# Kernel optimization log

Measured on AMD Instinct MI355X. Metric: run time of the kernel, lower is better.

The kernel has to match this reference:

```python
import jax, jax.numpy as jnp
import numpy as np

LENGTHSCALE = 0.3
EPS = 1e-10
N = 100000   # evaluation points
M = 3375     # grid_size**3 RBF centers


def setup_inputs() -> dict:
    key = jax.random.key(0)
    k1, k2, k3, k4, k5 = jax.random.split(key, 5)
    x = jax.random.normal(k1, (N, 3), dtype=jnp.float32)
    centers = jax.random.normal(k2, (M, 3), dtype=jnp.float32)
    coeff_u = jax.random.normal(k3, (M,), dtype=jnp.float32)
    coeff_v = jax.random.normal(k4, (M,), dtype=jnp.float32)
    coeff_w = jax.random.normal(k5, (M,), dtype=jnp.float32)
    return {"x": x, "centers": centers, "coeff_u": coeff_u,
            "coeff_v": coeff_v, "coeff_w": coeff_w}


def reference(x, centers, coeff_u, coeff_v, coeff_w):
    # base sphere-attractor field: x * (1 - ||x||)
    r = jnp.linalg.norm(x, axis=-1, keepdims=True)          # (N, 1)
    base = x * (1.0 - r)                                    # (N, 3)

    x_sq = jnp.sum(x * x, axis=-1, keepdims=True)           # (N, 1)
    c_sq = jnp.sum(centers * centers, axis=-1)[None, :]     # (1, M)
    xy = x @ centers.T                                      # (N, M)
    dist2 = jnp.maximum(x_sq + c_sq - 2.0 * xy, EPS)        # (N, M)

    # RBF features and three shared-phi matvecs fused as one matmul
    phi = jnp.exp(-dist2 / (2.0 * LENGTHSCALE ** 2))        # (N, M)
    coeffs = jnp.stack([coeff_u, coeff_v, coeff_w], axis=1) # (M, 3)
    uvw = phi @ coeffs                                      # (N, 3)
    return base + uvw
```

## Files before the change

kernel.cpp:

```cpp
#include <hip/hip_runtime.h>
#include <hip/hip_bf16.h>

#define S2 8.014973f
#define K2 16.029946f
#define NCHUNK 21

typedef float f2 __attribute__((ext_vector_type(2)));

__global__ void rbf_prep_kernel(const float* __restrict__ centers,
                                const float* __restrict__ cu,
                                const float* __restrict__ cv,
                                const float* __restrict__ cw,
                                float4* __restrict__ cpack, int M) {
    int m = blockIdx.x * 256 + threadIdx.x;
    if (m < M) {
        float cx = centers[3 * m + 0];
        float cy = centers[3 * m + 1];
        float cz = centers[3 * m + 2];
        float4 a, b;
        a.x = K2 * cx;
        a.y = K2 * cy;
        a.z = K2 * cz;
        a.w = -S2 * (cx * cx + cy * cy + cz * cz);
        b.x = cu[m];
        b.y = cv[m];
        b.z = cw[m];
        b.w = 0.f;
        cpack[2 * m + 0] = a;
        cpack[2 * m + 1] = b;
    }
}

__global__ __launch_bounds__(256) void rbf_main_kernel(
    const float* __restrict__ x, const float4* __restrict__ cpack,
    float* __restrict__ out, int N, int M, int NT, int per, int ntask) {
    const int tid = threadIdx.x;
    const int lane = tid & 63;
    const int wave0 =
        __builtin_amdgcn_readfirstlane(blockIdx.x * 4 + (tid >> 6));
    const int nwaves = gridDim.x * 4;

    for (int task = wave0; task < ntask; task += nwaves) {
        const int tile = task % NT;
        const int chunk = task / NT;
        const int p0 = tile * 128 + lane;
        const int p1 = p0 + 64;

        float x00 = 0.f, x01 = 0.f, x02 = 0.f;
        float x10 = 0.f, x11 = 0.f, x12 = 0.f;
        if (p0 < N) {
            x00 = x[3 * p0 + 0];
            x01 = x[3 * p0 + 1];
            x02 = x[3 * p0 + 2];
        }
        if (p1 < N) {
            x10 = x[3 * p1 + 0];
            x11 = x[3 * p1 + 1];
            x12 = x[3 * p1 + 2];
        }

        const f2 X = {x00, x10};
        const f2 Y = {x01, x11};
        const f2 Z = {x02, x12};
        const f2 PX = {-S2 * (x00 * x00 + x01 * x01 + x02 * x02),
                       -S2 * (x10 * x10 + x11 * x11 + x12 * x12)};

        const int jb = chunk * per;
        const int je = min(jb + per, M);

        f2 au = {0.f, 0.f}, av = {0.f, 0.f}, aw = {0.f, 0.f};

#pragma unroll 4
        for (int j = jb; j < je; ++j) {
            const float4 a = cpack[2 * j + 0];
            const float4 b = cpack[2 * j + 1];
            f2 e = PX + a.w;
            e += Z * a.z;
            e += Y * a.y;
            e += X * a.x;
            f2 phi;
            phi.x = __builtin_amdgcn_exp2f(e.x);
            phi.y = __builtin_amdgcn_exp2f(e.y);
            au += phi * b.x;
            av += phi * b.y;
            aw += phi * b.z;
        }

        if (chunk == 0) {
            float g0 = 1.f - sqrtf(x00 * x00 + x01 * x01 + x02 * x02);
            au.x += x00 * g0;
            av.x += x01 * g0;
            aw.x += x02 * g0;
            float g1 = 1.f - sqrtf(x10 * x10 + x11 * x11 + x12 * x12);
            au.y += x10 * g1;
            av.y += x11 * g1;
            aw.y += x12 * g1;
        }

        if (p0 < N) {
            atomicAdd(&out[3 * p0 + 0], au.x);
            atomicAdd(&out[3 * p0 + 1], av.x);
            atomicAdd(&out[3 * p0 + 2], aw.x);
        }
        if (p1 < N) {
            atomicAdd(&out[3 * p1 + 0], au.y);
            atomicAdd(&out[3 * p1 + 1], av.y);
            atomicAdd(&out[3 * p1 + 2], aw.y);
        }
    }
}

extern "C" void kernel_launch(void* const* d_in, const int* in_sizes, int n_in,
                              void* d_out, int out_size, void* d_ws,
                              size_t ws_size, hipStream_t stream) {
    const float* x = (const float*)d_in[0];
    const float* centers = (const float*)d_in[1];
    const float* cu = (const float*)d_in[2];
    const float* cv = (const float*)d_in[3];
    const float* cw = (const float*)d_in[4];
    const int N = in_sizes[0] / 3;
    const int M = in_sizes[1] / 3;
    float4* cpack = (float4*)d_ws;
    float* out = (float*)d_out;

    const int NT = (N + 127) / 128;
    const int per = (M + NCHUNK - 1) / NCHUNK;
    const int ntask = NT * NCHUNK;

    hipLaunchKernelGGL(rbf_prep_kernel, dim3((M + 255) / 256), dim3(256), 0,
                       stream, centers, cu, cv, cw, cpack, M);
    hipMemsetAsync(d_out, 0, (size_t)out_size * sizeof(float), stream);
    hipLaunchKernelGGL(rbf_main_kernel, dim3(2048), dim3(256), 0, stream, x,
                       cpack, out, N, M, NT, per, ntask);
}
```

Measured before the change: 146.8 us.

## Load center data via scalar prefetch and process four points per lane

Replaces per-lane vector loads of the packed center data with inline-asm scalar s_load_dwordx16, double-buffered so the next pair of centers loads while the current pair is computed. Each lane now handles four evaluation points instead of two, spreading every center load over more work. The center array is zero-padded to a fixed chunk size, so the inner loop has a compile-time trip count with no bounds checks. The costs are hand-written waitcnt handling, which is fragile against compiler scheduling, and a hard-coded PER constant that only covers the given M.

```diff
diff --git a/kernel.cpp b/kernel.cpp
--- a/kernel.cpp
+++ b/kernel.cpp
@@ -4,8 +4,10 @@
 #define S2 8.014973f
 #define K2 16.029946f
 #define NCHUNK 21
+#define PER 162
+#define MPAD (NCHUNK * PER)
 
-typedef float f2 __attribute__((ext_vector_type(2)));
+typedef float f16v __attribute__((ext_vector_type(16)));
 
 __global__ void rbf_prep_kernel(const float* __restrict__ centers,
                                 const float* __restrict__ cu,
@@ -13,19 +15,20 @@
                                 const float* __restrict__ cw,
                                 float4* __restrict__ cpack, int M) {
     int m = blockIdx.x * 256 + threadIdx.x;
-    if (m < M) {
-        float cx = centers[3 * m + 0];
-        float cy = centers[3 * m + 1];
-        float cz = centers[3 * m + 2];
-        float4 a, b;
-        a.x = K2 * cx;
-        a.y = K2 * cy;
-        a.z = K2 * cz;
-        a.w = -S2 * (cx * cx + cy * cy + cz * cz);
-        b.x = cu[m];
-        b.y = cv[m];
-        b.z = cw[m];
-        b.w = 0.f;
+    if (m < MPAD + 2) {
+        float4 a = {0.f, 0.f, 0.f, 0.f}, b = {0.f, 0.f, 0.f, 0.f};
+        if (m < M) {
+            float cx = centers[3 * m + 0];
+            float cy = centers[3 * m + 1];
+            float cz = centers[3 * m + 2];
+            a.x = K2 * cx;
+            a.y = K2 * cy;
+            a.z = K2 * cz;
+            a.w = -S2 * (cx * cx + cy * cy + cz * cz);
+            b.x = cu[m];
+            b.y = cv[m];
+            b.z = cw[m];
+        }
         cpack[2 * m + 0] = a;
         cpack[2 * m + 1] = b;
     }
@@ -33,79 +36,82 @@
 
 __global__ __launch_bounds__(256) void rbf_main_kernel(
     const float* __restrict__ x, const float4* __restrict__ cpack,
-    float* __restrict__ out, int N, int M, int NT, int per, int ntask) {
-    const int tid = threadIdx.x;
-    const int lane = tid & 63;
-    const int wave0 =
-        __builtin_amdgcn_readfirstlane(blockIdx.x * 4 + (tid >> 6));
+    float* __restrict__ out, int N, int NT, int ntask) {
+    const int lane = threadIdx.x & 63;
+    const int wid =
+        __builtin_amdgcn_readfirstlane(blockIdx.x * 4 + (threadIdx.x >> 6));
     const int nwaves = gridDim.x * 4;
 
-    for (int task = wave0; task < ntask; task += nwaves) {
+    for (int task = wid; task < ntask; task += nwaves) {
         const int tile = task % NT;
         const int chunk = task / NT;
-        const int p0 = tile * 128 + lane;
-        const int p1 = p0 + 64;
 
-        float x00 = 0.f, x01 = 0.f, x02 = 0.f;
-        float x10 = 0.f, x11 = 0.f, x12 = 0.f;
-        if (p0 < N) {
-            x00 = x[3 * p0 + 0];
-            x01 = x[3 * p0 + 1];
-            x02 = x[3 * p0 + 2];
+        float X[4], Y[4], Z[4], PX[4];
+        int p[4];
+#pragma unroll
+        for (int q = 0; q < 4; ++q) {
+            int pp = tile * 256 + q * 64 + lane;
+            p[q] = pp;
+            float a = 0.f, b = 0.f, c = 0.f;
+            if (pp < N) {
+                a = x[3 * pp + 0];
+                b = x[3 * pp + 1];
+                c = x[3 * pp + 2];
+            }
+            X[q] = a;
+            Y[q] = b;
+            Z[q] = c;
+            PX[q] = -S2 * (a * a + b * b + c * c);
         }
-        if (p1 < N) {
-            x10 = x[3 * p1 + 0];
-            x11 = x[3 * p1 + 1];
-            x12 = x[3 * p1 + 2];
-        }
+        float AU[4] = {0.f, 0.f, 0.f, 0.f};
+        float AV[4] = {0.f, 0.f, 0.f, 0.f};
+        float AW[4] = {0.f, 0.f, 0.f, 0.f};
 
-        const f2 X = {x00, x10};
-        const f2 Y = {x01, x11};
-        const f2 Z = {x02, x12};
-        const f2 PX = {-S2 * (x00 * x00 + x01 * x01 + x02 * x02),
-                       -S2 * (x10 * x10 + x11 * x11 + x12 * x12)};
-
-        const int jb = chunk * per;
-        const int je = min(jb + per, M);
-
-        f2 au = {0.f, 0.f}, av = {0.f, 0.f}, aw = {0.f, 0.f};
-
-#pragma unroll 4
-        for (int j = jb; j < je; ++j) {
-            const float4 a = cpack[2 * j + 0];
-            const float4 b = cpack[2 * j + 1];
-            f2 e = PX + a.w;
-            e += Z * a.z;
-            e += Y * a.y;
-            e += X * a.x;
-            f2 phi;
-            phi.x = __builtin_amdgcn_exp2f(e.x);
-            phi.y = __builtin_amdgcn_exp2f(e.y);
-            au += phi * b.x;
-            av += phi * b.y;
-            aw += phi * b.z;
+        uint64_t ap = (uint64_t)(const void*)(cpack + 2 * (size_t)chunk * PER);
+        f16v cc, cn;
+        asm volatile("s_load_dwordx16 %0, %1, 0x0" : "=s"(cc) : "s"(ap));
+        asm volatile("s_waitcnt lgkmcnt(0)" : "+s"(cc));
+#pragma unroll 1
+        for (int it = 0; it < PER / 2; ++it) {
+            ap += 64;
+            asm volatile("s_load_dwordx16 %0, %1, 0x0" : "=s"(cn) : "s"(ap));
+#pragma unroll
+            for (int q = 0; q < 4; ++q) {
+                float e0 = fmaf(X[q], cc[0],
+                           fmaf(Y[q], cc[1],
+                           fmaf(Z[q], cc[2], PX[q] + cc[3])));
+                float f0 = __builtin_amdgcn_exp2f(e0);
+                AU[q] = fmaf(f0, cc[4], AU[q]);
+                AV[q] = fmaf(f0, cc[5], AV[q]);
+                AW[q] = fmaf(f0, cc[6], AW[q]);
+                float e1 = fmaf(X[q], cc[8],
+                           fmaf(Y[q], cc[9],
+                           fmaf(Z[q], cc[10], PX[q] + cc[11])));
+                float f1 = __builtin_amdgcn_exp2f(e1);
+                AU[q] = fmaf(f1, cc[12], AU[q]);
+                AV[q] = fmaf(f1, cc[13], AV[q]);
+                AW[q] = fmaf(f1, cc[14], AW[q]);
+            }
+            asm volatile("s_waitcnt lgkmcnt(0)" : "+s"(cn));
+            cc = cn;
         }
 
         if (chunk == 0) {
-            float g0 = 1.f - sqrtf(x00 * x00 + x01 * x01 + x02 * x02);
-            au.x += x00 * g0;
-            av.x += x01 * g0;
-            aw.x += x02 * g0;
-            float g1 = 1.f - sqrtf(x10 * x10 + x11 * x11 + x12 * x12);
-            au.y += x10 * g1;
-            av.y += x11 * g1;
-            aw.y += x12 * g1;
+#pragma unroll
+            for (int q = 0; q < 4; ++q) {
+                float g = 1.f - sqrtf(X[q] * X[q] + Y[q] * Y[q] + Z[q] * Z[q]);
+                AU[q] += X[q] * g;
+                AV[q] += Y[q] * g;
+                AW[q] += Z[q] * g;
+            }
         }
-
-        if (p0 < N) {
-            atomicAdd(&out[3 * p0 + 0], au.x);
-            atomicAdd(&out[3 * p0 + 1], av.x);
-            atomicAdd(&out[3 * p0 + 2], aw.x);
-        }
-        if (p1 < N) {
-            atomicAdd(&out[3 * p1 + 0], au.y);
-            atomicAdd(&out[3 * p1 + 1], av.y);
-            atomicAdd(&out[3 * p1 + 2], aw.y);
+#pragma unroll
+        for (int q = 0; q < 4; ++q) {
+            if (p[q] < N) {
+                atomicAdd(&out[3 * p[q] + 0], AU[q]);
+                atomicAdd(&out[3 * p[q] + 1], AV[q]);
+                atomicAdd(&out[3 * p[q] + 2], AW[q]);
+            }
         }
     }
 }
@@ -123,13 +129,12 @@
     float4* cpack = (float4*)d_ws;
     float* out = (float*)d_out;
 
-    const int NT = (N + 127) / 128;
-    const int per = (M + NCHUNK - 1) / NCHUNK;
+    const int NT = (N + 255) / 256;
     const int ntask = NT * NCHUNK;
 
-    hipLaunchKernelGGL(rbf_prep_kernel, dim3((M + 255) / 256), dim3(256), 0,
-                       stream, centers, cu, cv, cw, cpack, M);
+    hipLaunchKernelGGL(rbf_prep_kernel, dim3((MPAD + 2 + 255) / 256), dim3(256),
+                       0, stream, centers, cu, cv, cw, cpack, M);
     hipMemsetAsync(d_out, 0, (size_t)out_size * sizeof(float), stream);
     hipLaunchKernelGGL(rbf_main_kernel, dim3(2048), dim3(256), 0, stream, x,
-                       cpack, out, N, M, NT, per, ntask);
+                       cpack, out, N, NT, ntask);
 }
```

New measurement: 158.4 us. +7.9%, slower.
